# Optimization experiments

Hardware: AMD Instinct MI355X
Metric: run time of the kernel (lower is better)

## Reference

```python
import jax, jax.numpy as jnp
import numpy as np

MARGIN = 0.3
HARD_FACTOR = 0.0
EPS = 1e-6


def setup_inputs() -> dict:
    key = jax.random.key(0)
    k1, k2 = jax.random.split(key)
    inputs = jax.random.normal(k1, (4096, 256), dtype=jnp.float32)
    targets = jax.random.randint(k2, (4096,), 0, 512, dtype=jnp.int64)
    return {"inputs": inputs, "targets": targets}


def reference(inputs, targets):
    n = inputs.shape[0]
    half = n // 2
    # L2-normalize features (matches normalize(): x / (||x|| + 1e-6))
    x = inputs / (jnp.linalg.norm(inputs, axis=-1, keepdims=True) + EPS)
    # pairwise euclidean distances, clamped at 1e-6 before sqrt
    sq = jnp.sum(x * x, axis=1)                      # (n,)
    dist = sq[:, None] + sq[None, :] - 2.0 * (x @ x.T)  # (n, n)
    dist = jnp.sqrt(jnp.clip(dist, EPS))
    # same-identity mask
    mask = targets[:, None] == targets[None, :]      # (n, n) bool
    # rows in the first half mine over columns [half:n], rows in the
    # second half mine over columns [0:half] -> gather the opposite half
    first = (jnp.arange(n) < half)[:, None]          # (n, 1)
    d_o = jnp.where(first, dist[:, half:], dist[:, :half])  # (n, half)
    m_o = jnp.where(first, mask[:, half:], mask[:, :half])  # (n, half) bool
    pos_any = jnp.any(m_o, axis=1)
    neg_any = jnp.any(~m_o, axis=1)
    dist_ap = jnp.where(pos_any,
                        jnp.max(jnp.where(m_o, d_o, -jnp.inf), axis=1),
                        0.0)
    dist_an = jnp.where(neg_any,
                        jnp.min(jnp.where(m_o, jnp.inf, d_o), axis=1),
                        1.0)
    dist_ap = dist_ap * (1.0 + HARD_FACTOR)
    dist_an = dist_an * (1.0 - HARD_FACTOR)
    # MarginRankingLoss(margin)(dist_an, dist_ap, y=1) =
    #   mean(relu(-(dist_an - dist_ap) + margin))
    loss = jnp.mean(jax.nn.relu(dist_ap - dist_an + MARGIN))
    return loss
```

## Files before the change

kernel.cpp:

```cpp
#include <hip/hip_runtime.h>
#include <hip/hip_bf16.h>
#include <math.h>

#define N 4096
#define D 256
#define HALF 2048
#define MARGIN 0.3f

#define BM 64
#define BK 32
#define LDB 40

typedef __attribute__((ext_vector_type(8))) short bf16x8;
typedef __attribute__((ext_vector_type(4))) float f32x4;

__global__ __launch_bounds__(256) void k_norm(const float* __restrict__ in,
                                              unsigned short* __restrict__ xnb,
                                              float* __restrict__ sq,
                                              int* __restrict__ ap,
                                              int* __restrict__ an) {
    const int row = blockIdx.x;
    const int t = threadIdx.x;
    float v = in[(size_t)row * D + t];
    float s = v * v;
#pragma unroll
    for (int o = 32; o > 0; o >>= 1) s += __shfl_down(s, o, 64);
    __shared__ float wsum[4];
    __shared__ float inv_s, sq_s;
    if ((t & 63) == 0) wsum[t >> 6] = s;
    __syncthreads();
    if (t == 0) {
        float tot = wsum[0] + wsum[1] + wsum[2] + wsum[3];
        float nrm = sqrtf(tot);
        float inv = 1.0f / (nrm + 1e-6f);
        inv_s = inv;
        float q = nrm * inv;
        sq_s = q * q;
    }
    __syncthreads();
    float x = v * inv_s;
    unsigned int u = __float_as_uint(x);
    xnb[(size_t)row * D + t] =
        (unsigned short)((u + 0x7fffu + ((u >> 16) & 1u)) >> 16);
    if (t == 0) {
        sq[row] = sq_s;
        ap[row] = 0;
        an[row] = 0x7f800000;
    }
}

__global__ __launch_bounds__(256) void k_tile(const unsigned short* __restrict__ xnb,
                                              const float* __restrict__ sq,
                                              const int* __restrict__ tg,
                                              int* __restrict__ ap,
                                              int* __restrict__ an) {
    __shared__ unsigned short As[BM * LDB];
    __shared__ unsigned short Bs[BM * LDB];
    __shared__ int sra[BM], srn[BM], sca[BM], scn[BM];

    const int bi = blockIdx.y, bj = blockIdx.x;
    const int I0 = bi * BM;
    const int J0 = bj * BM;
    const int tid = threadIdx.x;
    const int wave = tid >> 6, lane = tid & 63;
    const int wm = wave >> 1, wn = wave & 1;
    const int lrow = lane & 15, lquad = lane >> 4;

    f32x4 acc[2][2];
#pragma unroll
    for (int a = 0; a < 2; ++a)
#pragma unroll
        for (int b = 0; b < 2; ++b) acc[a][b] = (f32x4){0.f, 0.f, 0.f, 0.f};

    const unsigned short* Ag = xnb + (size_t)I0 * D;
    const unsigned short* Bg = xnb + (size_t)(HALF + J0) * D;
    const int srow = tid >> 2, sseg = tid & 3;

    for (int k0 = 0; k0 < D; k0 += BK) {
        __syncthreads();
        *(uint4*)&As[srow * LDB + sseg * 8] =
            *(const uint4*)&Ag[(size_t)srow * D + k0 + sseg * 8];
        *(uint4*)&Bs[srow * LDB + sseg * 8] =
            *(const uint4*)&Bg[(size_t)srow * D + k0 + sseg * 8];
        __syncthreads();
        bf16x8 af[2], bfr[2];
#pragma unroll
        for (int mi = 0; mi < 2; ++mi)
            af[mi] = *(const bf16x8*)&As[(wm * 32 + mi * 16 + lrow) * LDB + lquad * 8];
#pragma unroll
        for (int nj = 0; nj < 2; ++nj)
            bfr[nj] = *(const bf16x8*)&Bs[(wn * 32 + nj * 16 + lrow) * LDB + lquad * 8];
#pragma unroll
        for (int mi = 0; mi < 2; ++mi)
#pragma unroll
            for (int nj = 0; nj < 2; ++nj)
                acc[mi][nj] = __builtin_amdgcn_mfma_f32_16x16x32_bf16(
                    af[mi], bfr[nj], acc[mi][nj], 0, 0, 0);
    }

    float sqi[2][4], sqj[2];
    int tgi[2][4], tgj[2];
#pragma unroll
    for (int mi = 0; mi < 2; ++mi)
#pragma unroll
        for (int r = 0; r < 4; ++r) {
            int gi = I0 + wm * 32 + mi * 16 + lquad * 4 + r;
            sqi[mi][r] = sq[gi];
            tgi[mi][r] = tg[gi];
        }
#pragma unroll
    for (int nj = 0; nj < 2; ++nj) {
        int gj = HALF + J0 + wn * 32 + nj * 16 + lrow;
        sqj[nj] = sq[gj];
        tgj[nj] = tg[gj];
    }

    const float INF = __int_as_float(0x7f800000);
    float rap[2][4], ran[2][4], capv[2], canv[2];
#pragma unroll
    for (int mi = 0; mi < 2; ++mi)
#pragma unroll
        for (int r = 0; r < 4; ++r) { rap[mi][r] = 0.f; ran[mi][r] = INF; }
#pragma unroll
    for (int nj = 0; nj < 2; ++nj) { capv[nj] = 0.f; canv[nj] = INF; }

#pragma unroll
    for (int mi = 0; mi < 2; ++mi)
#pragma unroll
        for (int nj = 0; nj < 2; ++nj)
#pragma unroll
            for (int r = 0; r < 4; ++r) {
                float d2 = sqi[mi][r] + sqj[nj] - 2.0f * acc[mi][nj][r];
                float d = sqrtf(fmaxf(d2, 1e-6f));
                if (tgi[mi][r] == tgj[nj]) {
                    rap[mi][r] = fmaxf(rap[mi][r], d);
                    capv[nj] = fmaxf(capv[nj], d);
                } else {
                    ran[mi][r] = fminf(ran[mi][r], d);
                    canv[nj] = fminf(canv[nj], d);
                }
            }

#pragma unroll
    for (int mi = 0; mi < 2; ++mi)
#pragma unroll
        for (int r = 0; r < 4; ++r) {
#pragma unroll
            for (int o = 1; o < 16; o <<= 1) {
                rap[mi][r] = fmaxf(rap[mi][r], __shfl_xor(rap[mi][r], o, 64));
                ran[mi][r] = fminf(ran[mi][r], __shfl_xor(ran[mi][r], o, 64));
            }
        }
#pragma unroll
    for (int nj = 0; nj < 2; ++nj) {
#pragma unroll
        for (int o = 16; o < 64; o <<= 1) {
            capv[nj] = fmaxf(capv[nj], __shfl_xor(capv[nj], o, 64));
            canv[nj] = fminf(canv[nj], __shfl_xor(canv[nj], o, 64));
        }
    }

    if (tid < BM) { sra[tid] = 0; srn[tid] = 0x7f800000;
                    sca[tid] = 0; scn[tid] = 0x7f800000; }
    __syncthreads();
    if (lrow == 0) {
#pragma unroll
        for (int mi = 0; mi < 2; ++mi)
#pragma unroll
            for (int r = 0; r < 4; ++r) {
                int lr = wm * 32 + mi * 16 + lquad * 4 + r;
                atomicMax(&sra[lr], __float_as_int(rap[mi][r]));
                atomicMin(&srn[lr], __float_as_int(ran[mi][r]));
            }
    }
    if (lquad == 0) {
#pragma unroll
        for (int nj = 0; nj < 2; ++nj) {
            int lc = wn * 32 + nj * 16 + lrow;
            atomicMax(&sca[lc], __float_as_int(capv[nj]));
            atomicMin(&scn[lc], __float_as_int(canv[nj]));
        }
    }
    __syncthreads();
    if (tid < BM) {
        atomicMax(&ap[I0 + tid], sra[tid]);
        atomicMin(&an[I0 + tid], srn[tid]);
        atomicMax(&ap[HALF + J0 + tid], sca[tid]);
        atomicMin(&an[HALF + J0 + tid], scn[tid]);
    }
}

__global__ __launch_bounds__(1024) void k_loss(const int* __restrict__ ap,
                                               const int* __restrict__ an,
                                               float* __restrict__ out) {
    const int t = threadIdx.x;
    float s = 0.f;
#pragma unroll
    for (int i = t; i < N; i += 1024) {
        float dap = __int_as_float(ap[i]);
        int anb = an[i];
        float dan = (anb == 0x7f800000) ? 1.0f : __int_as_float(anb);
        float v = dap - dan + MARGIN;
        s += (v > 0.f) ? v : 0.f;
    }
#pragma unroll
    for (int o = 32; o > 0; o >>= 1) s += __shfl_down(s, o, 64);
    __shared__ float wsum[16];
    if ((t & 63) == 0) wsum[t >> 6] = s;
    __syncthreads();
    if (t == 0) {
        float tot = 0.f;
#pragma unroll
        for (int w = 0; w < 16; ++w) tot += wsum[w];
        out[0] = tot / (float)N;
    }
}

extern "C" void kernel_launch(void* const* d_in, const int* in_sizes, int n_in,
                              void* d_out, int out_size, void* d_ws, size_t ws_size,
                              hipStream_t stream) {
    const float* in = (const float*)d_in[0];
    const int* tg = (const int*)d_in[1];
    float* out = (float*)d_out;

    unsigned short* xnb = (unsigned short*)d_ws;
    float* sq = (float*)(xnb + (size_t)N * D);
    int* ap = (int*)(sq + N);
    int* an = ap + N;

    k_norm<<<N, 256, 0, stream>>>(in, xnb, sq, ap, an);
    k_tile<<<dim3(HALF / BM, HALF / BM), 256, 0, stream>>>(xnb, sq, tg, ap, an);
    k_loss<<<1, 1024, 0, stream>>>(ap, an, out);
}
```

Baseline: 72.81 us.

## Fuse normalization into tile kernel and replace global atomics with partial-buffer reduction

Each 64x64 tile block now loads its own fp32 rows, normalizes them, converts them to bf16 straight into full-K shared memory, and runs all MFMAs without per-K-step syncs. The separate norm kernel and its workspace round trip are gone. Global atomicMax/Min is replaced by writing per-tile partial row and column results to buffers, which a two-stage reduce kernel then combines. In exchange, every block redoes normalization of 128 rows (32x redundant global reads of the fp32 input) and uses more shared memory per block.

```diff
diff --git a/kernel.cpp b/kernel.cpp
--- a/kernel.cpp
+++ b/kernel.cpp
@@ -1,5 +1,4 @@
 #include <hip/hip_runtime.h>
-#include <hip/hip_bf16.h>
 #include <math.h>
 
 #define N 4096
@@ -8,54 +7,26 @@
 #define MARGIN 0.3f
 
 #define BM 64
-#define BK 32
-#define LDB 40
+#define LDA 264
+#define NTB (HALF/BM)
 
 typedef __attribute__((ext_vector_type(8))) short bf16x8;
 typedef __attribute__((ext_vector_type(4))) float f32x4;
 
-__global__ __launch_bounds__(256) void k_norm(const float* __restrict__ in,
-                                              unsigned short* __restrict__ xnb,
-                                              float* __restrict__ sq,
-                                              int* __restrict__ ap,
-                                              int* __restrict__ an) {
-    const int row = blockIdx.x;
-    const int t = threadIdx.x;
-    float v = in[(size_t)row * D + t];
-    float s = v * v;
-#pragma unroll
-    for (int o = 32; o > 0; o >>= 1) s += __shfl_down(s, o, 64);
-    __shared__ float wsum[4];
-    __shared__ float inv_s, sq_s;
-    if ((t & 63) == 0) wsum[t >> 6] = s;
-    __syncthreads();
-    if (t == 0) {
-        float tot = wsum[0] + wsum[1] + wsum[2] + wsum[3];
-        float nrm = sqrtf(tot);
-        float inv = 1.0f / (nrm + 1e-6f);
-        inv_s = inv;
-        float q = nrm * inv;
-        sq_s = q * q;
-    }
-    __syncthreads();
-    float x = v * inv_s;
+__device__ __forceinline__ unsigned short bf16_rne(float x) {
     unsigned int u = __float_as_uint(x);
-    xnb[(size_t)row * D + t] =
-        (unsigned short)((u + 0x7fffu + ((u >> 16) & 1u)) >> 16);
-    if (t == 0) {
-        sq[row] = sq_s;
-        ap[row] = 0;
-        an[row] = 0x7f800000;
-    }
-}
-
-__global__ __launch_bounds__(256) void k_tile(const unsigned short* __restrict__ xnb,
-                                              const float* __restrict__ sq,
-                                              const int* __restrict__ tg,
-                                              int* __restrict__ ap,
-                                              int* __restrict__ an) {
-    __shared__ unsigned short As[BM * LDB];
-    __shared__ unsigned short Bs[BM * LDB];
+    return (unsigned short)((u + 0x7fffu + ((u >> 16) & 1u)) >> 16);
+}
+
+__global__ __launch_bounds__(256) void k_fused(const float* __restrict__ in,
+                                               const int* __restrict__ tg,
+                                               float* __restrict__ rowap,
+                                               float* __restrict__ rowan,
+                                               float* __restrict__ colap,
+                                               float* __restrict__ colan) {
+    __shared__ unsigned short As[BM * LDA];
+    __shared__ unsigned short Bs[BM * LDA];
+    __shared__ float sqv[128];
     __shared__ int sra[BM], srn[BM], sca[BM], scn[BM];
 
     const int bi = blockIdx.y, bj = blockIdx.x;
@@ -66,30 +37,46 @@
     const int wm = wave >> 1, wn = wave & 1;
     const int lrow = lane & 15, lquad = lane >> 4;
 
+#pragma unroll 4
+    for (int it = 0; it < 32; ++it) {
+        int rr = wave * 32 + it;
+        int g = (rr < 64) ? (I0 + rr) : (HALF + J0 + (rr - 64));
+        float4 v = *(const float4*)&in[(size_t)g * D + lane * 4];
+        float s = v.x * v.x + v.y * v.y + v.z * v.z + v.w * v.w;
+#pragma unroll
+        for (int o = 1; o < 64; o <<= 1) s += __shfl_xor(s, o, 64);
+        float nrm = sqrtf(s);
+        float inv = 1.0f / (nrm + 1e-6f);
+        ushort4 h;
+        h.x = bf16_rne(v.x * inv);
+        h.y = bf16_rne(v.y * inv);
+        h.z = bf16_rne(v.z * inv);
+        h.w = bf16_rne(v.w * inv);
+        unsigned short* dst = (rr < 64) ? &As[rr * LDA + lane * 4]
+                                        : &Bs[(rr - 64) * LDA + lane * 4];
+        *(ushort4*)dst = h;
+        if (lane == 0) {
+            float q = nrm * inv;
+            sqv[rr] = q * q;
+        }
+    }
+    __syncthreads();
+
     f32x4 acc[2][2];
 #pragma unroll
     for (int a = 0; a < 2; ++a)
 #pragma unroll
         for (int b = 0; b < 2; ++b) acc[a][b] = (f32x4){0.f, 0.f, 0.f, 0.f};
 
-    const unsigned short* Ag = xnb + (size_t)I0 * D;
-    const unsigned short* Bg = xnb + (size_t)(HALF + J0) * D;
-    const int srow = tid >> 2, sseg = tid & 3;
-
-    for (int k0 = 0; k0 < D; k0 += BK) {
-        __syncthreads();
-        *(uint4*)&As[srow * LDB + sseg * 8] =
-            *(const uint4*)&Ag[(size_t)srow * D + k0 + sseg * 8];
-        *(uint4*)&Bs[srow * LDB + sseg * 8] =
-            *(const uint4*)&Bg[(size_t)srow * D + k0 + sseg * 8];
-        __syncthreads();
+#pragma unroll
+    for (int k0 = 0; k0 < D; k0 += 32) {
         bf16x8 af[2], bfr[2];
 #pragma unroll
         for (int mi = 0; mi < 2; ++mi)
-            af[mi] = *(const bf16x8*)&As[(wm * 32 + mi * 16 + lrow) * LDB + lquad * 8];
+            af[mi] = *(const bf16x8*)&As[(wm * 32 + mi * 16 + lrow) * LDA + k0 + lquad * 8];
 #pragma unroll
         for (int nj = 0; nj < 2; ++nj)
-            bfr[nj] = *(const bf16x8*)&Bs[(wn * 32 + nj * 16 + lrow) * LDB + lquad * 8];
+            bfr[nj] = *(const bf16x8*)&Bs[(wn * 32 + nj * 16 + lrow) * LDA + k0 + lquad * 8];
 #pragma unroll
         for (int mi = 0; mi < 2; ++mi)
 #pragma unroll
@@ -104,15 +91,15 @@
     for (int mi = 0; mi < 2; ++mi)
 #pragma unroll
         for (int r = 0; r < 4; ++r) {
-            int gi = I0 + wm * 32 + mi * 16 + lquad * 4 + r;
-            sqi[mi][r] = sq[gi];
-            tgi[mi][r] = tg[gi];
+            int lr = wm * 32 + mi * 16 + lquad * 4 + r;
+            sqi[mi][r] = sqv[lr];
+            tgi[mi][r] = tg[I0 + lr];
         }
 #pragma unroll
     for (int nj = 0; nj < 2; ++nj) {
-        int gj = HALF + J0 + wn * 32 + nj * 16 + lrow;
-        sqj[nj] = sq[gj];
-        tgj[nj] = tg[gj];
+        int lc = wn * 32 + nj * 16 + lrow;
+        sqj[nj] = sqv[64 + lc];
+        tgj[nj] = tg[HALF + J0 + lc];
     }
 
     const float INF = __int_as_float(0x7f800000);
@@ -144,21 +131,19 @@
 #pragma unroll
     for (int mi = 0; mi < 2; ++mi)
 #pragma unroll
-        for (int r = 0; r < 4; ++r) {
+        for (int r = 0; r < 4; ++r)
 #pragma unroll
             for (int o = 1; o < 16; o <<= 1) {
                 rap[mi][r] = fmaxf(rap[mi][r], __shfl_xor(rap[mi][r], o, 64));
                 ran[mi][r] = fminf(ran[mi][r], __shfl_xor(ran[mi][r], o, 64));
             }
-        }
-#pragma unroll
-    for (int nj = 0; nj < 2; ++nj) {
+#pragma unroll
+    for (int nj = 0; nj < 2; ++nj)
 #pragma unroll
         for (int o = 16; o < 64; o <<= 1) {
             capv[nj] = fmaxf(capv[nj], __shfl_xor(capv[nj], o, 64));
             canv[nj] = fminf(canv[nj], __shfl_xor(canv[nj], o, 64));
         }
-    }
 
     if (tid < BM) { sra[tid] = 0; srn[tid] = 0x7f800000;
                     sca[tid] = 0; scn[tid] = 0x7f800000; }
@@ -183,35 +168,52 @@
     }
     __syncthreads();
     if (tid < BM) {
-        atomicMax(&ap[I0 + tid], sra[tid]);
-        atomicMin(&an[I0 + tid], srn[tid]);
-        atomicMax(&ap[HALF + J0 + tid], sca[tid]);
-        atomicMin(&an[HALF + J0 + tid], scn[tid]);
-    }
-}
-
-__global__ __launch_bounds__(1024) void k_loss(const int* __restrict__ ap,
-                                               const int* __restrict__ an,
-                                               float* __restrict__ out) {
+        rowap[bj * HALF + I0 + tid] = __int_as_float(sra[tid]);
+        rowan[bj * HALF + I0 + tid] = __int_as_float(srn[tid]);
+        colap[bi * HALF + J0 + tid] = __int_as_float(sca[tid]);
+        colan[bi * HALF + J0 + tid] = __int_as_float(scn[tid]);
+    }
+}
+
+__global__ __launch_bounds__(256) void k_reduce(const float* __restrict__ rowap,
+                                                const float* __restrict__ rowan,
+                                                const float* __restrict__ colap,
+                                                const float* __restrict__ colan,
+                                                float* __restrict__ bsum) {
     const int t = threadIdx.x;
-    float s = 0.f;
-#pragma unroll
-    for (int i = t; i < N; i += 1024) {
-        float dap = __int_as_float(ap[i]);
-        int anb = an[i];
-        float dan = (anb == 0x7f800000) ? 1.0f : __int_as_float(anb);
-        float v = dap - dan + MARGIN;
-        s += (v > 0.f) ? v : 0.f;
-    }
+    const int gid = blockIdx.x * 256 + t;
+    const float INF = __int_as_float(0x7f800000);
+    float ap = 0.f, an = INF;
+    if (gid < HALF) {
+#pragma unroll
+        for (int b = 0; b < NTB; ++b) {
+            ap = fmaxf(ap, rowap[b * HALF + gid]);
+            an = fminf(an, rowan[b * HALF + gid]);
+        }
+    } else {
+        int j = gid - HALF;
+#pragma unroll
+        for (int b = 0; b < NTB; ++b) {
+            ap = fmaxf(ap, colap[b * HALF + j]);
+            an = fminf(an, colan[b * HALF + j]);
+        }
+    }
+    if (an == INF) an = 1.0f;
+    float v = ap - an + MARGIN;
+    float s = (v > 0.f) ? v : 0.f;
 #pragma unroll
     for (int o = 32; o > 0; o >>= 1) s += __shfl_down(s, o, 64);
-    __shared__ float wsum[16];
+    __shared__ float wsum[4];
     if ((t & 63) == 0) wsum[t >> 6] = s;
     __syncthreads();
-    if (t == 0) {
+    if (t == 0) bsum[blockIdx.x] = wsum[0] + wsum[1] + wsum[2] + wsum[3];
+}
+
+__global__ void k_final(const float* __restrict__ bsum, float* __restrict__ out) {
+    if (threadIdx.x == 0) {
         float tot = 0.f;
 #pragma unroll
-        for (int w = 0; w < 16; ++w) tot += wsum[w];
+        for (int b = 0; b < 16; ++b) tot += bsum[b];
         out[0] = tot / (float)N;
     }
 }
@@ -223,12 +225,13 @@
     const int* tg = (const int*)d_in[1];
     float* out = (float*)d_out;
 
-    unsigned short* xnb = (unsigned short*)d_ws;
-    float* sq = (float*)(xnb + (size_t)N * D);
-    int* ap = (int*)(sq + N);
-    int* an = ap + N;
-
-    k_norm<<<N, 256, 0, stream>>>(in, xnb, sq, ap, an);
-    k_tile<<<dim3(HALF / BM, HALF / BM), 256, 0, stream>>>(xnb, sq, tg, ap, an);
-    k_loss<<<1, 1024, 0, stream>>>(ap, an, out);
-}
+    float* rowap = (float*)d_ws;
+    float* rowan = rowap + NTB * HALF;
+    float* colap = rowan + NTB * HALF;
+    float* colan = colap + NTB * HALF;
+    float* bsum  = colan + NTB * HALF;
+
+    k_fused<<<dim3(NTB, NTB), 256, 0, stream>>>(in, tg, rowap, rowan, colap, colan);
+    k_reduce<<<16, 256, 0, stream>>>(rowap, rowan, colap, colan, bsum);
+    k_final<<<1, 64, 0, stream>>>(bsum, out);
+}
```

Result: slower. 114.3 us (+56.9%).
